# Kernel tuning notes

Hardware: AMD Instinct MI355X
Metric: run time of the kernel (lower is better)

The kernel has to match this reference:

```python
import jax, jax.numpy as jnp
import numpy as np

IN_CH, D, K = 256, 128, 512

def setup_inputs() -> dict:
    key = jax.random.key(0)
    k1, k2, k3, k4 = jax.random.split(key, 4)
    x = jax.random.normal(k1, (16, IN_CH, 64, 64), dtype=jnp.float32)
    W = jax.random.normal(k2, (D, IN_CH), dtype=jnp.float32) * (1.0 / np.sqrt(IN_CH))
    b = jax.random.normal(k3, (D,), dtype=jnp.float32) * 0.01
    prototypes = jax.random.normal(k4, (K, D), dtype=jnp.float32) * 0.02
    gamma = jnp.asarray(1.0, dtype=jnp.float32)
    return {"x": x, "W": W, "b": b, "prototypes": prototypes, "gamma": gamma}

def reference(x, W, b, prototypes, gamma):
    n, c, h, w = x.shape
    # 1x1 conv projection: [n,c,h,w] -> [n,h,w,d]
    q = jnp.einsum('nchw,dc->nhwd', x, W) + b
    q_flat = q.reshape(n * h * w, -1)                      # [T, d]
    q_norm2 = jnp.sum(q_flat * q_flat, axis=1, keepdims=True)   # [T, 1]
    p_norm2 = jnp.sum(prototypes * prototypes, axis=1)[None, :] # [1, K]
    dist2 = q_norm2 + p_norm2 - 2.0 * (q_flat @ prototypes.T)   # [T, K]
    weights = jax.nn.softmax(-jnp.abs(gamma) * dist2, axis=1)
    return weights.reshape(n, h, w, -1).transpose(0, 3, 1, 2)   # [n, K, h, w]
```

## Files before the change

kernel.cpp:

```cpp
#include <hip/hip_runtime.h>

#define HW 4096
#define NCH 256
#define DIM 128
#define NPROTO 512

typedef __attribute__((ext_vector_type(4))) float f32x4;
typedef __attribute__((ext_vector_type(8))) short s16x8;
typedef __attribute__((ext_vector_type(4))) unsigned u32x4;

__device__ __forceinline__ unsigned short f2bf(float f) {
  union { float f; unsigned u; } v; v.f = f;
  unsigned r = v.u + 0x7fffu + ((v.u >> 16) & 1u);
  return (unsigned short)(r >> 16);
}

__global__ __launch_bounds__(256) void prep_kernel(const float* __restrict__ P,
                                                   const float* __restrict__ Wm,
                                                   unsigned short* __restrict__ Pr,
                                                   unsigned short* __restrict__ Wr,
                                                   float* __restrict__ pn2) {
  const int tid = threadIdx.x;
  if (blockIdx.x < 8) {
    const int n  = blockIdx.x * 64 + (tid >> 2);
    const int qt = tid & 3;
    const float* row = P + n * DIM + qt * 32;
    unsigned short* dst = Pr + ((size_t)qt * NPROTO + n) * 32;
    float ssq = 0.f;
#pragma unroll
    for (int u = 0; u < 8; ++u) {
      f32x4 v = *(const f32x4*)(row + 4 * u);
      ssq += v.x * v.x + v.y * v.y + v.z * v.z + v.w * v.w;
      dst[4 * u + 0] = f2bf(v.x);
      dst[4 * u + 1] = f2bf(v.y);
      dst[4 * u + 2] = f2bf(v.z);
      dst[4 * u + 3] = f2bf(v.w);
    }
    ssq += __shfl_xor(ssq, 1);
    ssq += __shfl_xor(ssq, 2);
    if (qt == 0) pn2[n] = ssq;
  } else {
#pragma unroll
    for (int it = 0; it < 2; ++it) {
      const int p  = (blockIdx.x - 8) * 256 + tid + 512 * it;
      const int d  = p >> 3;
      const int ch = p & 7;
      const float* src = Wm + d * NCH + 32 * ch;
      unsigned short* dst = Wr + ((size_t)ch * DIM + d) * 32;
#pragma unroll
      for (int u = 0; u < 8; ++u) {
        f32x4 v = *(const f32x4*)(src + 4 * u);
        dst[4 * u + 0] = f2bf(v.x);
        dst[4 * u + 1] = f2bf(v.y);
        dst[4 * u + 2] = f2bf(v.z);
        dst[4 * u + 3] = f2bf(v.w);
      }
    }
  }
}

__global__ __launch_bounds__(512, 2) void proj_kernel(const float* __restrict__ x,
                                                      const unsigned short* __restrict__ Wr,
                                                      const float* __restrict__ bias,
                                                      unsigned short* __restrict__ qbf) {
  __shared__ __align__(16) unsigned short x_s[2][128 * 40];
  const int tid  = threadIdx.x;
  const int p0   = blockIdx.x * 128;
  const int nimg = p0 >> 12;
  const int hw0  = p0 & 4095;
  const float* xbase = x + (size_t)nimg * NCH * HW + hw0;
  const int wave = tid >> 6, lane = tid & 63;
  const int l15 = lane & 15, l4 = lane >> 4;
  const int pix = tid & 127;
  const int qq  = tid >> 7;

  f32x4 acc[8];
#pragma unroll
  for (int j = 0; j < 8; ++j)
#pragma unroll
    for (int r = 0; r < 4; ++r) acc[j][r] = 0.f;

  {
    const float* src = xbase + (size_t)(8 * qq) * HW + pix;
    u32x4 vv;
#pragma unroll
    for (int jj = 0; jj < 4; ++jj) {
      float f0 = src[(size_t)(2 * jj) * HW];
      float f1 = src[(size_t)(2 * jj + 1) * HW];
      vv[jj] = (unsigned)f2bf(f0) | ((unsigned)f2bf(f1) << 16);
    }
    *(u32x4*)&x_s[0][pix * 40 + 8 * qq] = vv;
  }
  __syncthreads();

  const int m = 16 * wave + l15;
  for (int ch = 0; ch < 8; ++ch) {
    if (ch < 7) {
      const float* src = xbase + (size_t)(32 * (ch + 1) + 8 * qq) * HW + pix;
      u32x4 vv;
#pragma unroll
      for (int jj = 0; jj < 4; ++jj) {
        float f0 = src[(size_t)(2 * jj) * HW];
        float f1 = src[(size_t)(2 * jj + 1) * HW];
        vv[jj] = (unsigned)f2bf(f0) | ((unsigned)f2bf(f1) << 16);
      }
      *(u32x4*)&x_s[(ch + 1) & 1][pix * 40 + 8 * qq] = vv;
    }
    s16x8 a = *(const s16x8*)&x_s[ch & 1][m * 40 + 8 * l4];
    const unsigned short* wbase = Wr + ((size_t)ch * DIM + l15) * 32 + 8 * l4;
#pragma unroll
    for (int j = 0; j < 8; ++j) {
      s16x8 b = *(const s16x8*)(wbase + (size_t)(16 * j) * 32);
      acc[j] = __builtin_amdgcn_mfma_f32_16x16x32_bf16(a, b, acc[j], 0, 0, 0);
    }
    __syncthreads();
  }

  const int mb = 16 * wave + 4 * l4;
#pragma unroll
  for (int j = 0; j < 8; ++j) {
    const int d = 16 * j + l15;
    const float bv = bias[d];
#pragma unroll
    for (int r = 0; r < 4; ++r)
      qbf[(size_t)(p0 + mb + r) * DIM + d] = f2bf(acc[j][r] + bv);
  }
}

__global__ __launch_bounds__(512) void attn_kernel(const unsigned short* __restrict__ qbf,
                                                   const unsigned short* __restrict__ Pr,
                                                   const float* __restrict__ pn2,
                                                   const float* __restrict__ gptr,
                                                   float* __restrict__ out) {
  __shared__ __align__(16) unsigned short q_s[64 * 136];
  float* red  = (float*)q_s;
  float* rmx  = (float*)q_s + 512;
  float* rinv = (float*)q_s + 576;

  const int tid  = threadIdx.x;
  const int p0   = blockIdx.x * 64;
  const int nimg = p0 >> 12;
  const int hw0  = p0 & 4095;
  const int wave = tid >> 6, lane = tid & 63;
  const int l15 = lane & 15, l4 = lane >> 4;
  const float g = fabsf(gptr[0]);

  {
    const int r = tid >> 3, c8 = tid & 7;
#pragma unroll
    for (int it = 0; it < 2; ++it) {
      const int col = c8 + 8 * it;
      s16x8 v = *(const s16x8*)(qbf + (size_t)(p0 + r) * DIM + 8 * col);
      *(s16x8*)&q_s[r * 136 + 8 * col] = v;
    }
  }
  __syncthreads();

  f32x4 acc[4][4];
#pragma unroll
  for (int i = 0; i < 4; ++i)
#pragma unroll
    for (int j = 0; j < 4; ++j)
#pragma unroll
      for (int r = 0; r < 4; ++r) acc[i][j][r] = 0.f;

#pragma unroll
  for (int ch = 0; ch < 4; ++ch) {
    s16x8 afr[4];
#pragma unroll
    for (int i = 0; i < 4; ++i)
      afr[i] = *(const s16x8*)&q_s[(16 * i + l15) * 136 + 32 * ch + 8 * l4];
    const unsigned short* pb = Pr + ((size_t)ch * NPROTO + 64 * wave + l15) * 32 + 8 * l4;
#pragma unroll
    for (int j = 0; j < 4; ++j) {
      s16x8 bfr = *(const s16x8*)(pb + (size_t)(16 * j) * 32);
#pragma unroll
      for (int i = 0; i < 4; ++i)
        acc[i][j] = __builtin_amdgcn_mfma_f32_16x16x32_bf16(afr[i], bfr, acc[i][j], 0, 0, 0);
    }
  }
  __syncthreads();

  float pnv[4];
#pragma unroll
  for (int j = 0; j < 4; ++j) pnv[j] = pn2[64 * wave + 16 * j + l15];

#pragma unroll
  for (int i = 0; i < 4; ++i)
#pragma unroll
    for (int r = 0; r < 4; ++r) {
      float m = -1e30f;
#pragma unroll
      for (int j = 0; j < 4; ++j) {
        float lv = g * (2.f * acc[i][j][r] - pnv[j]);
        acc[i][j][r] = lv;
        m = fmaxf(m, lv);
      }
#pragma unroll
      for (int s = 1; s < 16; s <<= 1) m = fmaxf(m, __shfl_xor(m, s));
      if (l15 == 0) red[wave * 64 + 16 * i + 4 * l4 + r] = m;
    }
  __syncthreads();
  if (tid < 64) {
    float M = red[tid];
#pragma unroll
    for (int w = 1; w < 8; ++w) M = fmaxf(M, red[w * 64 + tid]);
    rmx[tid] = M;
  }
  __syncthreads();

#pragma unroll
  for (int i = 0; i < 4; ++i)
#pragma unroll
    for (int r = 0; r < 4; ++r) {
      const float M = rmx[16 * i + 4 * l4 + r];
      float s = 0.f;
#pragma unroll
      for (int j = 0; j < 4; ++j) {
        float e = __expf(acc[i][j][r] - M);
        acc[i][j][r] = e;
        s += e;
      }
#pragma unroll
      for (int t = 1; t < 16; t <<= 1) s += __shfl_xor(s, t);
      if (l15 == 0) red[wave * 64 + 16 * i + 4 * l4 + r] = s;
    }
  __syncthreads();
  if (tid < 64) {
    float S = 0.f;
#pragma unroll
    for (int w = 0; w < 8; ++w) S += red[w * 64 + tid];
    rinv[tid] = 1.f / S;
  }
  __syncthreads();

  float inv[4][4];
#pragma unroll
  for (int i = 0; i < 4; ++i)
#pragma unroll
    for (int r = 0; r < 4; ++r) inv[i][r] = rinv[16 * i + 4 * l4 + r];

  const size_t outbase = (size_t)nimg * NPROTO * HW + hw0;
#pragma unroll
  for (int j = 0; j < 4; ++j) {
    float* op = out + outbase + (size_t)(64 * wave + 16 * j + l15) * HW + 4 * l4;
#pragma unroll
    for (int i = 0; i < 4; ++i) {
      f32x4 o;
#pragma unroll
      for (int r = 0; r < 4; ++r) o[r] = acc[i][j][r] * inv[i][r];
      *(f32x4*)(op + 16 * i) = o;
    }
  }
}

extern "C" void kernel_launch(void* const* d_in, const int* in_sizes, int n_in,
                              void* d_out, int out_size, void* d_ws, size_t ws_size,
                              hipStream_t stream) {
  const float* x     = (const float*)d_in[0];
  const float* Wm    = (const float*)d_in[1];
  const float* bias  = (const float*)d_in[2];
  const float* prot  = (const float*)d_in[3];
  const float* gamma = (const float*)d_in[4];
  float* out = (float*)d_out;

  unsigned short* q_ws  = (unsigned short*)d_ws;
  unsigned short* P_ws  = (unsigned short*)((char*)d_ws + 16777216);
  unsigned short* W_ws  = (unsigned short*)((char*)d_ws + 16777216 + 131072);
  float*          pn2_w = (float*)((char*)d_ws + 16777216 + 131072 + 65536);

  prep_kernel<<<10, 256, 0, stream>>>(prot, Wm, P_ws, W_ws, pn2_w);
  proj_kernel<<<512, 512, 0, stream>>>(x, W_ws, bias, q_ws);
  attn_kernel<<<1024, 512, 0, stream>>>(q_ws, P_ws, pn2_w, gamma, out);
}
```

Measured before the change: 248.3 us.

## Fuse projection and prototype softmax into one kernel keeping q in LDS

Merges the 1x1-conv projection kernel and the distance/softmax kernel into one kernel that handles 32 pixels per block. Each block loads its x tile with vectorized reads into an XOR-swizzled LDS layout, computes q with MFMA, and keeps q in LDS instead of writing bf16 q to a global workspace and reading it back. This removes the global q round-trip and one kernel launch. In exchange, tiles are smaller, so prototype fragments are reloaded from global or L2 by twice as many blocks, and each block has less MFMA work to amortize the loads.

After: 232.9 us. 6.2% less time.

```diff
diff --git a/kernel.cpp b/kernel.cpp
--- a/kernel.cpp
+++ b/kernel.cpp
@@ -7,7 +7,8 @@
 
 typedef __attribute__((ext_vector_type(4))) float f32x4;
 typedef __attribute__((ext_vector_type(8))) short s16x8;
-typedef __attribute__((ext_vector_type(4))) unsigned u32x4;
+typedef __attribute__((ext_vector_type(4))) short s16x4;
+typedef __attribute__((ext_vector_type(2))) unsigned u32x2;
 
 __device__ __forceinline__ unsigned short f2bf(float f) {
   union { float f; unsigned u; } v; v.f = f;
@@ -59,86 +60,22 @@
   }
 }
 
-__global__ __launch_bounds__(512, 2) void proj_kernel(const float* __restrict__ x,
-                                                      const unsigned short* __restrict__ Wr,
-                                                      const float* __restrict__ bias,
-                                                      unsigned short* __restrict__ qbf) {
-  __shared__ __align__(16) unsigned short x_s[2][128 * 40];
+__global__ __launch_bounds__(512) void fused_kernel(const float* __restrict__ x,
+                                                    const unsigned short* __restrict__ Wr,
+                                                    const float* __restrict__ bias,
+                                                    const unsigned short* __restrict__ Pr,
+                                                    const float* __restrict__ pn2,
+                                                    const float* __restrict__ gptr,
+                                                    float* __restrict__ out) {
+  __shared__ __align__(16) char smem[25088];
+  unsigned short* x_s = (unsigned short*)smem;
+  unsigned short* q_s = (unsigned short*)(smem + 16384);
+  float* red  = (float*)smem;
+  float* rmx  = (float*)smem + 256;
+  float* rinv = (float*)smem + 288;
+
   const int tid  = threadIdx.x;
-  const int p0   = blockIdx.x * 128;
-  const int nimg = p0 >> 12;
-  const int hw0  = p0 & 4095;
-  const float* xbase = x + (size_t)nimg * NCH * HW + hw0;
-  const int wave = tid >> 6, lane = tid & 63;
-  const int l15 = lane & 15, l4 = lane >> 4;
-  const int pix = tid & 127;
-  const int qq  = tid >> 7;
-
-  f32x4 acc[8];
-#pragma unroll
-  for (int j = 0; j < 8; ++j)
-#pragma unroll
-    for (int r = 0; r < 4; ++r) acc[j][r] = 0.f;
-
-  {
-    const float* src = xbase + (size_t)(8 * qq) * HW + pix;
-    u32x4 vv;
-#pragma unroll
-    for (int jj = 0; jj < 4; ++jj) {
-      float f0 = src[(size_t)(2 * jj) * HW];
-      float f1 = src[(size_t)(2 * jj + 1) * HW];
-      vv[jj] = (unsigned)f2bf(f0) | ((unsigned)f2bf(f1) << 16);
-    }
-    *(u32x4*)&x_s[0][pix * 40 + 8 * qq] = vv;
-  }
-  __syncthreads();
-
-  const int m = 16 * wave + l15;
-  for (int ch = 0; ch < 8; ++ch) {
-    if (ch < 7) {
-      const float* src = xbase + (size_t)(32 * (ch + 1) + 8 * qq) * HW + pix;
-      u32x4 vv;
-#pragma unroll
-      for (int jj = 0; jj < 4; ++jj) {
-        float f0 = src[(size_t)(2 * jj) * HW];
-        float f1 = src[(size_t)(2 * jj + 1) * HW];
-        vv[jj] = (unsigned)f2bf(f0) | ((unsigned)f2bf(f1) << 16);
-      }
-      *(u32x4*)&x_s[(ch + 1) & 1][pix * 40 + 8 * qq] = vv;
-    }
-    s16x8 a = *(const s16x8*)&x_s[ch & 1][m * 40 + 8 * l4];
-    const unsigned short* wbase = Wr + ((size_t)ch * DIM + l15) * 32 + 8 * l4;
-#pragma unroll
-    for (int j = 0; j < 8; ++j) {
-      s16x8 b = *(const s16x8*)(wbase + (size_t)(16 * j) * 32);
-      acc[j] = __builtin_amdgcn_mfma_f32_16x16x32_bf16(a, b, acc[j], 0, 0, 0);
-    }
-    __syncthreads();
-  }
-
-  const int mb = 16 * wave + 4 * l4;
-#pragma unroll
-  for (int j = 0; j < 8; ++j) {
-    const int d = 16 * j + l15;
-    const float bv = bias[d];
-#pragma unroll
-    for (int r = 0; r < 4; ++r)
-      qbf[(size_t)(p0 + mb + r) * DIM + d] = f2bf(acc[j][r] + bv);
-  }
-}
-
-__global__ __launch_bounds__(512) void attn_kernel(const unsigned short* __restrict__ qbf,
-                                                   const unsigned short* __restrict__ Pr,
-                                                   const float* __restrict__ pn2,
-                                                   const float* __restrict__ gptr,
-                                                   float* __restrict__ out) {
-  __shared__ __align__(16) unsigned short q_s[64 * 136];
-  float* red  = (float*)q_s;
-  float* rmx  = (float*)q_s + 512;
-  float* rinv = (float*)q_s + 576;
-
-  const int tid  = threadIdx.x;
-  const int p0   = blockIdx.x * 64;
+  const int p0   = blockIdx.x * 32;
   const int nimg = p0 >> 12;
   const int hw0  = p0 & 4095;
   const int wave = tid >> 6, lane = tid & 63;
@@ -146,47 +83,87 @@
   const float g = fabsf(gptr[0]);
 
   {
-    const int r = tid >> 3, c8 = tid & 7;
-#pragma unroll
-    for (int it = 0; it < 2; ++it) {
-      const int col = c8 + 8 * it;
-      s16x8 v = *(const s16x8*)(qbf + (size_t)(p0 + r) * DIM + 8 * col);
-      *(s16x8*)&q_s[r * 136 + 8 * col] = v;
-    }
-  }
-  __syncthreads();
-
-  f32x4 acc[4][4];
-#pragma unroll
-  for (int i = 0; i < 4; ++i)
+    const int f  = tid & 7;
+    const int gg = (tid >> 3) & 31;
+    const int h  = tid >> 8;
+    const float* src = x + (size_t)nimg * NCH * HW + hw0
+                         + (size_t)(8 * gg + 4 * h) * HW + 4 * f;
+    f32x4 v0 = *(const f32x4*)(src);
+    f32x4 v1 = *(const f32x4*)(src + HW);
+    f32x4 v2 = *(const f32x4*)(src + 2 * HW);
+    f32x4 v3 = *(const f32x4*)(src + 3 * HW);
+#pragma unroll
+    for (int j = 0; j < 4; ++j) {
+      const int pix  = 4 * f + j;
+      const int slot = (gg & 24) | ((gg ^ (pix >> 1)) & 7);
+      u32x2 wv;
+      wv.x = (unsigned)f2bf(v0[j]) | ((unsigned)f2bf(v1[j]) << 16);
+      wv.y = (unsigned)f2bf(v2[j]) | ((unsigned)f2bf(v3[j]) << 16);
+      *(u32x2*)(x_s + pix * 256 + slot * 8 + 4 * h) = wv;
+    }
+  }
+  __syncthreads();
+
+  {
+    const int mtb  = (wave & 3) * 2;
+    const int nt   = wave >> 2;
+    const int pixb = 16 * nt + l15;
+    f32x4 qa0 = {0.f, 0.f, 0.f, 0.f};
+    f32x4 qa1 = {0.f, 0.f, 0.f, 0.f};
+#pragma unroll
+    for (int kc = 0; kc < 8; ++kc) {
+      const int gb   = 4 * kc + l4;
+      const int slot = (gb & 24) | ((gb ^ (pixb >> 1)) & 7);
+      s16x8 xb = *(const s16x8*)(x_s + pixb * 256 + slot * 8);
+      const unsigned short* wb = Wr + (size_t)(kc * DIM + l15) * 32 + 8 * l4;
+      s16x8 w0 = *(const s16x8*)(wb + (size_t)(16 * mtb) * 32);
+      s16x8 w1 = *(const s16x8*)(wb + (size_t)(16 * (mtb + 1)) * 32);
+      qa0 = __builtin_amdgcn_mfma_f32_16x16x32_bf16(w0, xb, qa0, 0, 0, 0);
+      qa1 = __builtin_amdgcn_mfma_f32_16x16x32_bf16(w1, xb, qa1, 0, 0, 0);
+    }
+#pragma unroll
+    for (int mm = 0; mm < 2; ++mm) {
+      const int d0 = 16 * (mtb + mm) + 4 * l4;
+      f32x4 qa = mm ? qa1 : qa0;
+      f32x4 bv = *(const f32x4*)(bias + d0);
+      s16x4 o;
+#pragma unroll
+      for (int r = 0; r < 4; ++r) o[r] = (short)f2bf(qa[r] + bv[r]);
+      *(s16x4*)(q_s + pixb * 136 + d0) = o;
+    }
+  }
+  __syncthreads();
+
+  f32x4 acc[2][4];
+#pragma unroll
+  for (int i = 0; i < 2; ++i)
 #pragma unroll
     for (int j = 0; j < 4; ++j)
 #pragma unroll
       for (int r = 0; r < 4; ++r) acc[i][j][r] = 0.f;
 
 #pragma unroll
-  for (int ch = 0; ch < 4; ++ch) {
-    s16x8 afr[4];
-#pragma unroll
-    for (int i = 0; i < 4; ++i)
-      afr[i] = *(const s16x8*)&q_s[(16 * i + l15) * 136 + 32 * ch + 8 * l4];
-    const unsigned short* pb = Pr + ((size_t)ch * NPROTO + 64 * wave + l15) * 32 + 8 * l4;
+  for (int kc = 0; kc < 4; ++kc) {
+    s16x8 afr[2];
+#pragma unroll
+    for (int i = 0; i < 2; ++i)
+      afr[i] = *(const s16x8*)(q_s + (16 * i + l15) * 136 + 32 * kc + 8 * l4);
+    const unsigned short* pb = Pr + (size_t)(kc * NPROTO + 64 * wave + l15) * 32 + 8 * l4;
 #pragma unroll
     for (int j = 0; j < 4; ++j) {
       s16x8 bfr = *(const s16x8*)(pb + (size_t)(16 * j) * 32);
 #pragma unroll
-      for (int i = 0; i < 4; ++i)
+      for (int i = 0; i < 2; ++i)
         acc[i][j] = __builtin_amdgcn_mfma_f32_16x16x32_bf16(afr[i], bfr, acc[i][j], 0, 0, 0);
     }
   }
-  __syncthreads();
 
   float pnv[4];
 #pragma unroll
   for (int j = 0; j < 4; ++j) pnv[j] = pn2[64 * wave + 16 * j + l15];
 
 #pragma unroll
-  for (int i = 0; i < 4; ++i)
+  for (int i = 0; i < 2; ++i)
 #pragma unroll
     for (int r = 0; r < 4; ++r) {
       float m = -1e30f;
@@ -198,19 +175,19 @@
       }
 #pragma unroll
       for (int s = 1; s < 16; s <<= 1) m = fmaxf(m, __shfl_xor(m, s));
-      if (l15 == 0) red[wave * 64 + 16 * i + 4 * l4 + r] = m;
-    }
-  __syncthreads();
-  if (tid < 64) {
+      if (l15 == 0) red[wave * 32 + 16 * i + 4 * l4 + r] = m;
+    }
+  __syncthreads();
+  if (tid < 32) {
     float M = red[tid];
 #pragma unroll
-    for (int w = 1; w < 8; ++w) M = fmaxf(M, red[w * 64 + tid]);
+    for (int w = 1; w < 8; ++w) M = fmaxf(M, red[w * 32 + tid]);
     rmx[tid] = M;
   }
   __syncthreads();
 
 #pragma unroll
-  for (int i = 0; i < 4; ++i)
+  for (int i = 0; i < 2; ++i)
 #pragma unroll
     for (int r = 0; r < 4; ++r) {
       const float M = rmx[16 * i + 4 * l4 + r];
@@ -223,20 +200,20 @@
       }
 #pragma unroll
       for (int t = 1; t < 16; t <<= 1) s += __shfl_xor(s, t);
-      if (l15 == 0) red[wave * 64 + 16 * i + 4 * l4 + r] = s;
-    }
-  __syncthreads();
-  if (tid < 64) {
+      if (l15 == 0) red[wave * 32 + 16 * i + 4 * l4 + r] = s;
+    }
+  __syncthreads();
+  if (tid < 32) {
     float S = 0.f;
 #pragma unroll
-    for (int w = 0; w < 8; ++w) S += red[w * 64 + tid];
+    for (int w = 0; w < 8; ++w) S += red[w * 32 + tid];
     rinv[tid] = 1.f / S;
   }
   __syncthreads();
 
-  float inv[4][4];
-#pragma unroll
-  for (int i = 0; i < 4; ++i)
+  float inv[2][4];
+#pragma unroll
+  for (int i = 0; i < 2; ++i)
 #pragma unroll
     for (int r = 0; r < 4; ++r) inv[i][r] = rinv[16 * i + 4 * l4 + r];
 
@@ -245,7 +222,7 @@
   for (int j = 0; j < 4; ++j) {
     float* op = out + outbase + (size_t)(64 * wave + 16 * j + l15) * HW + 4 * l4;
 #pragma unroll
-    for (int i = 0; i < 4; ++i) {
+    for (int i = 0; i < 2; ++i) {
       f32x4 o;
 #pragma unroll
       for (int r = 0; r < 4; ++r) o[r] = acc[i][j][r] * inv[i][r];
@@ -264,12 +241,10 @@
   const float* gamma = (const float*)d_in[4];
   float* out = (float*)d_out;
 
-  unsigned short* q_ws  = (unsigned short*)d_ws;
-  unsigned short* P_ws  = (unsigned short*)((char*)d_ws + 16777216);
-  unsigned short* W_ws  = (unsigned short*)((char*)d_ws + 16777216 + 131072);
-  float*          pn2_w = (float*)((char*)d_ws + 16777216 + 131072 + 65536);
+  unsigned short* P_ws  = (unsigned short*)d_ws;
+  unsigned short* W_ws  = (unsigned short*)((char*)d_ws + 131072);
+  float*          pn2_w = (float*)((char*)d_ws + 131072 + 65536);
 
   prep_kernel<<<10, 256, 0, stream>>>(prot, Wm, P_ws, W_ws, pn2_w);
-  proj_kernel<<<512, 512, 0, stream>>>(x, W_ws, bias, q_ws);
-  attn_kernel<<<1024, 512, 0, stream>>>(q_ws, P_ws, pn2_w, gamma, out);
-}
+  fused_kernel<<<2048, 512, 0, stream>>>(x, W_ws, bias, P_ws, pn2_w, gamma, out);
+}
```
